# Performance work log

Hardware: AMD Instinct MI355X
Metric: run time of the kernel (lower is better)

## Reference

```python
import jax, jax.numpy as jnp
import numpy as np

FIELD_DIMS = [1000000, 100000, 1008, 1004, 102, 1000, 500, 50, 112, 107]
B = 16384
EMB = 32
DENSE = 16
MLP = [256, 128, 64]
BN_EPS = 1e-5
V_TOTAL = int(np.sum(FIELD_DIMS))
OFFSETS = jnp.asarray(np.concatenate([[0], np.cumsum(FIELD_DIMS)[:-1]]), dtype=jnp.int64)


def _xavier(key, fan_out, fan_in):
    lim = float(np.sqrt(6.0 / (fan_in + fan_out)))
    return jax.random.uniform(key, (fan_out, fan_in), jnp.float32, -lim, lim)


def setup_inputs() -> dict:
    key = jax.random.key(0)
    ks = jax.random.split(key, 16)
    # per-field in-range indices, stacked to [B, n_fields]
    sparse_cols = [jax.random.randint(jax.random.fold_in(ks[0], i), (B,), 0, d)
                   for i, d in enumerate(FIELD_DIMS)]
    sparse_inputs = jnp.stack(sparse_cols, axis=1).astype(jnp.int64)
    dense_inputs = jax.random.normal(ks[1], (B, DENSE), jnp.float32)
    # concatenated embedding / first-order bias tables (same math as per-field nn.Embedding)
    emb_table = 0.01 * jax.random.normal(ks[2], (V_TOTAL, EMB), jnp.float32)
    bias_table = 0.01 * jax.random.normal(ks[3], (V_TOTAL, 1), jnp.float32)
    fm_bias = jnp.zeros((1,), jnp.float32)
    dims = [len(FIELD_DIMS) * EMB + DENSE] + MLP
    params = {}
    for li in range(len(MLP)):
        params[f"W{li}"] = _xavier(ks[4 + li], dims[li + 1], dims[li])
        params[f"b{li}"] = jnp.zeros((dims[li + 1],), jnp.float32)
        params[f"g{li}"] = jnp.ones((dims[li + 1],), jnp.float32)
        params[f"be{li}"] = jnp.zeros((dims[li + 1],), jnp.float32)
    Wo = _xavier(ks[10], 1, MLP[-1])
    bo = jnp.zeros((1,), jnp.float32)
    return dict(sparse_inputs=sparse_inputs, dense_inputs=dense_inputs,
                emb_table=emb_table, bias_table=bias_table, fm_bias=fm_bias,
                Wo=Wo, bo=bo, **params)


def reference(sparse_inputs, dense_inputs, emb_table, bias_table, fm_bias,
              Wo, bo, W0, b0, g0, be0, W1, b1, g1, be1, W2, b2, g2, be2):
    idx = sparse_inputs + OFFSETS[None, :]           # [B, F] global rows
    field_embs = emb_table[idx]                      # [B, F, E] multi-table gather
    # FM first order: sum of per-field scalar biases
    fm_first = bias_table[idx][..., 0].sum(axis=1)   # [B]
    # FM second order: 0.5 * sum_d ((sum_f e)^2 - sum_f e^2)
    s = field_embs.sum(axis=1)                       # [B, E]
    sq = (field_embs * field_embs).sum(axis=1)       # [B, E]
    fm_second = 0.5 * (s * s - sq).sum(axis=-1)      # [B]
    fm_out = fm_bias[0] + fm_first + fm_second
    # deep component (BatchNorm in eval mode at init stats: mean=0, var=1; dropout=identity)
    x = jnp.concatenate([field_embs.reshape(field_embs.shape[0], -1), dense_inputs], axis=-1)
    inv = 1.0 / jnp.sqrt(1.0 + BN_EPS)
    for W, b, g, be in ((W0, b0, g0, be0), (W1, b1, g1, be1), (W2, b2, g2, be2)):
        h = x @ W.T + b
        h = h * (g * inv) + be
        x = jax.nn.relu(h)
    deep_out = (x @ Wo.T + bo)[:, 0]
    return jax.nn.sigmoid(fm_out + deep_out)
```

## Files before the change

### kernel.cpp

```cpp
#include <hip/hip_runtime.h>
#include <hip/hip_bf16.h>
#include <math.h>

#define BROWS 16384
#define NF    10
#define EMB   32
#define DENSE 16
#define K0S   352
#define K0    336
#define N0    256
#define N1    128
#define N2    64
#define BN_INV 0.99999500003749969f

__constant__ int c_offsets[NF] = {
    0, 1000000, 1100000, 1101008, 1102012,
    1102114, 1103114, 1103614, 1103664, 1103776
};

typedef short  bf16x8 __attribute__((ext_vector_type(8)));
typedef float  f32x4  __attribute__((ext_vector_type(4)));

union Frag { bf16x8 v; unsigned u[4]; };

static __device__ __forceinline__ unsigned short f2bf(float x) {
    union { float f; unsigned u; } c; c.f = x;
    unsigned r = (c.u + 0x7FFFu + ((c.u >> 16) & 1u)) >> 16;
    return (unsigned short)r;
}
static __device__ __forceinline__ unsigned pk2(float x, float y) {
    __hip_bfloat162 h = __float22bfloat162_rn(make_float2(x, y));
    union { __hip_bfloat162 h; unsigned u; } c; c.h = h; return c.u;
}

__global__ __launch_bounds__(256) void k_wconv_all(
    const float* __restrict__ W0, const float* __restrict__ W1,
    const float* __restrict__ W2,
    unsigned short* __restrict__ W0b, unsigned short* __restrict__ W1b,
    unsigned short* __restrict__ W2b)
{
    int i = blockIdx.x * 256 + threadIdx.x;
    if (i < N0 * K0S) {
        int r = i / K0S, c = i - r * K0S;
        W0b[i] = f2bf(c < K0 ? W0[r * K0 + c] : 0.f);
    } else if (i < N0 * K0S + N1 * N0) {
        int j = i - N0 * K0S;
        W1b[j] = f2bf(W1[j]);
    } else {
        int j = i - (N0 * K0S + N1 * N0);
        W2b[j] = f2bf(W2[j]);
    }
}

__global__ __launch_bounds__(256) void k_fused_all(
    const int*   __restrict__ sparse,
    const float* __restrict__ dense,
    const float* __restrict__ emb,
    const float* __restrict__ bias_tab,
    const float* __restrict__ fm_bias,
    const unsigned short* __restrict__ W0b,
    const float* __restrict__ b0, const float* __restrict__ g0,
    const float* __restrict__ be0,
    const unsigned short* __restrict__ W1b,
    const float* __restrict__ b1, const float* __restrict__ g1,
    const float* __restrict__ be1,
    const unsigned short* __restrict__ W2b,
    const float* __restrict__ b2, const float* __restrict__ g2,
    const float* __restrict__ be2,
    const float* __restrict__ Wo,
    const float* __restrict__ bo,
    float* __restrict__ out)
{
    __shared__ unsigned short x1s[32][N0 + 2];
    __shared__ unsigned short h2s[32][N1 + 2];
    __shared__ float fmld[32];
    __shared__ float partial[2][32];

    const int tid  = threadIdx.x;
    const int wave = tid >> 6;
    const int lane = tid & 63;
    const int l16  = lane & 15;
    const int quad = lane >> 4;
    const int rg   = wave & 1;
    const int hh   = wave >> 1;
    const int bm   = blockIdx.x * 32;
    const int arow = bm + rg * 16 + l16;

    int idx[NF];
#pragma unroll
    for (int f = 0; f < NF; ++f)
        idx[f] = sparse[arow * NF + f] + c_offsets[f];

    float first = 0.f, sq = 0.f;
    float s8[8];
#pragma unroll
    for (int j = 0; j < 8; ++j) s8[j] = 0.f;

    if (hh == 0) {
#pragma unroll
        for (int f = 0; f < NF; ++f)
            if ((f & 3) == quad) first += bias_tab[idx[f]];
    }

    f32x4 acc1[8];
#pragma unroll
    for (int nt = 0; nt < 8; ++nt) acc1[nt] = (f32x4){0.f, 0.f, 0.f, 0.f};

    const unsigned short* wp0 = W0b + (size_t)(hh * 128 + l16) * K0S + quad * 8;

#pragma unroll
    for (int f = 0; f < NF; ++f) {
        const float4* ep = (const float4*)(emb + (size_t)idx[f] * EMB) + quad * 2;
        float4 v0 = ep[0];
        float4 v1 = ep[1];
        if (hh == 0) {
            s8[0] += v0.x; s8[1] += v0.y; s8[2] += v0.z; s8[3] += v0.w;
            s8[4] += v1.x; s8[5] += v1.y; s8[6] += v1.z; s8[7] += v1.w;
            sq += v0.x*v0.x + v0.y*v0.y + v0.z*v0.z + v0.w*v0.w
                + v1.x*v1.x + v1.y*v1.y + v1.z*v1.z + v1.w*v1.w;
        }
        Frag a;
        a.u[0] = pk2(v0.x, v0.y); a.u[1] = pk2(v0.z, v0.w);
        a.u[2] = pk2(v1.x, v1.y); a.u[3] = pk2(v1.z, v1.w);
#pragma unroll
        for (int nt = 0; nt < 8; ++nt) {
            bf16x8 w = *(const bf16x8*)(wp0 + (size_t)(nt * 16) * K0S + f * 32);
            acc1[nt] = __builtin_amdgcn_mfma_f32_16x16x32_bf16(a.v, w, acc1[nt], 0, 0, 0);
        }
    }
    {
        Frag a;
        if (quad < 2) {
            const float4* dp = (const float4*)(dense + arow * DENSE) + quad * 2;
            float4 v0 = dp[0];
            float4 v1 = dp[1];
            a.u[0] = pk2(v0.x, v0.y); a.u[1] = pk2(v0.z, v0.w);
            a.u[2] = pk2(v1.x, v1.y); a.u[3] = pk2(v1.z, v1.w);
        } else {
            a.u[0] = 0; a.u[1] = 0; a.u[2] = 0; a.u[3] = 0;
        }
#pragma unroll
        for (int nt = 0; nt < 8; ++nt) {
            bf16x8 w = *(const bf16x8*)(wp0 + (size_t)(nt * 16) * K0S + 320);
            acc1[nt] = __builtin_amdgcn_mfma_f32_16x16x32_bf16(a.v, w, acc1[nt], 0, 0, 0);
        }
    }

    if (hh == 0) {
        float ss = 0.f;
#pragma unroll
        for (int j = 0; j < 8; ++j) ss += s8[j] * s8[j];
        ss += __shfl_xor(ss, 16); ss += __shfl_xor(ss, 32);
        sq += __shfl_xor(sq, 16); sq += __shfl_xor(sq, 32);
        first += __shfl_xor(first, 16); first += __shfl_xor(first, 32);
        if (quad == 0)
            fmld[rg * 16 + l16] = fm_bias[0] + first + 0.5f * (ss - sq);
    }

#pragma unroll
    for (int nt = 0; nt < 8; ++nt) {
        int col = hh * 128 + nt * 16 + l16;
        float sc = g0[col] * BN_INV;
        float tb = fmaf(b0[col], sc, be0[col]);
#pragma unroll
        for (int r = 0; r < 4; ++r) {
            float v = fmaf(acc1[nt][r], sc, tb);
            v = v > 0.f ? v : 0.f;
            x1s[rg * 16 + quad * 4 + r][col] = f2bf(v);
        }
    }
    __syncthreads();

    f32x4 acc2[4];
#pragma unroll
    for (int nt = 0; nt < 4; ++nt) acc2[nt] = (f32x4){0.f, 0.f, 0.f, 0.f};
    const unsigned short* wp1 = W1b + (size_t)(hh * 64 + l16) * N0 + quad * 8;
#pragma unroll
    for (int ks = 0; ks < 8; ++ks) {
        bf16x8 a = *(const bf16x8*)(&x1s[rg * 16 + l16][ks * 32 + quad * 8]);
#pragma unroll
        for (int nt = 0; nt < 4; ++nt) {
            bf16x8 w = *(const bf16x8*)(wp1 + (size_t)(nt * 16) * N0 + ks * 32);
            acc2[nt] = __builtin_amdgcn_mfma_f32_16x16x32_bf16(a, w, acc2[nt], 0, 0, 0);
        }
    }
#pragma unroll
    for (int nt = 0; nt < 4; ++nt) {
        int col = hh * 64 + nt * 16 + l16;
        float sc = g1[col] * BN_INV;
        float tb = fmaf(b1[col], sc, be1[col]);
#pragma unroll
        for (int r = 0; r < 4; ++r) {
            float v = fmaf(acc2[nt][r], sc, tb);
            v = v > 0.f ? v : 0.f;
            h2s[rg * 16 + quad * 4 + r][col] = f2bf(v);
        }
    }
    __syncthreads();

    f32x4 acc3[2];
#pragma unroll
    for (int nt = 0; nt < 2; ++nt) acc3[nt] = (f32x4){0.f, 0.f, 0.f, 0.f};
    const unsigned short* wp2 = W2b + (size_t)(hh * 32 + l16) * N1 + quad * 8;
#pragma unroll
    for (int ks = 0; ks < 4; ++ks) {
        bf16x8 a = *(const bf16x8*)(&h2s[rg * 16 + l16][ks * 32 + quad * 8]);
#pragma unroll
        for (int nt = 0; nt < 2; ++nt) {
            bf16x8 w = *(const bf16x8*)(wp2 + (size_t)(nt * 16) * N1 + ks * 32);
            acc3[nt] = __builtin_amdgcn_mfma_f32_16x16x32_bf16(a, w, acc3[nt], 0, 0, 0);
        }
    }

    float p[4] = {0.f, 0.f, 0.f, 0.f};
#pragma unroll
    for (int nt = 0; nt < 2; ++nt) {
        int col = hh * 32 + nt * 16 + l16;
        float sc = g2[col] * BN_INV;
        float tb = fmaf(b2[col], sc, be2[col]);
        float wo = Wo[col];
#pragma unroll
        for (int r = 0; r < 4; ++r) {
            float v = fmaf(acc3[nt][r], sc, tb);
            v = v > 0.f ? v : 0.f;
            p[r] = fmaf(v, wo, p[r]);
        }
    }
#pragma unroll
    for (int r = 0; r < 4; ++r) {
        p[r] += __shfl_xor(p[r], 1);
        p[r] += __shfl_xor(p[r], 2);
        p[r] += __shfl_xor(p[r], 4);
        p[r] += __shfl_xor(p[r], 8);
    }
    if (l16 == 0) {
#pragma unroll
        for (int r = 0; r < 4; ++r)
            partial[hh][rg * 16 + quad * 4 + r] = p[r];
    }
    __syncthreads();

    if (tid < 32) {
        float z = fmld[tid] + partial[0][tid] + partial[1][tid] + bo[0];
        out[bm + tid] = 1.f / (1.f + expf(-z));
    }
}

extern "C" void kernel_launch(void* const* d_in, const int* in_sizes, int n_in,
                              void* d_out, int out_size, void* d_ws, size_t ws_size,
                              hipStream_t stream)
{
    const int*   sparse   = (const int*)  d_in[0];
    const float* dense    = (const float*)d_in[1];
    const float* emb      = (const float*)d_in[2];
    const float* bias_tab = (const float*)d_in[3];
    const float* fm_bias  = (const float*)d_in[4];
    const float* Wo       = (const float*)d_in[5];
    const float* bo       = (const float*)d_in[6];
    const float* W0 = (const float*)d_in[7];
    const float* b0 = (const float*)d_in[8];
    const float* g0 = (const float*)d_in[9];
    const float* be0= (const float*)d_in[10];
    const float* W1 = (const float*)d_in[11];
    const float* b1 = (const float*)d_in[12];
    const float* g1 = (const float*)d_in[13];
    const float* be1= (const float*)d_in[14];
    const float* W2 = (const float*)d_in[15];
    const float* b2 = (const float*)d_in[16];
    const float* g2 = (const float*)d_in[17];
    const float* be2= (const float*)d_in[18];

    float* out = (float*)d_out;

    char* p = (char*)d_ws;
    unsigned short* W0b = (unsigned short*)p; p += (size_t)N0 * K0S * 2;
    unsigned short* W1b = (unsigned short*)p; p += (size_t)N1 * N0 * 2;
    unsigned short* W2b = (unsigned short*)p; p += (size_t)N2 * N1 * 2;

    k_wconv_all<<<(N0 * K0S + N1 * N0 + N2 * N1) / 256, 256, 0, stream>>>(
        W0, W1, W2, W0b, W1b, W2b);

    k_fused_all<<<BROWS / 32, 256, 0, stream>>>(
        sparse, dense, emb, bias_tab, fm_bias,
        W0b, b0, g0, be0, W1b, b1, g1, be1, W2b, b2, g2, be2,
        Wo, bo, out);
}
```

Before: 234.6 us.

## Stage gathered embeddings in LDS and split MLP columns across four waves

The block first gathers all 32 rows' embeddings into a shared bf16 A tile, using coalesced float4 loads driven by indices held in shared memory. The FM terms are then computed from that tile, and each of the four waves handles a quarter of the output columns for both 16-row groups. Before, two waves redundantly gathered the same embeddings and loaded disjoint halves of the weights. Now each embedding row is fetched once and each weight fragment is reused across 32 rows, at the cost of extra LDS traffic and syncs. The FM second-order term is now computed from bf16-rounded embeddings, which slightly reduces its precision.

New measurement: 230.9 us. Within noise of the previous version (-1.6%).

```diff
diff --git a/kernel.cpp b/kernel.cpp
--- a/kernel.cpp
+++ b/kernel.cpp
@@ -21,8 +21,6 @@
 typedef short  bf16x8 __attribute__((ext_vector_type(8)));
 typedef float  f32x4  __attribute__((ext_vector_type(4)));
 
-union Frag { bf16x8 v; unsigned u[4]; };
-
 static __device__ __forceinline__ unsigned short f2bf(float x) {
     union { float f; unsigned u; } c; c.f = x;
     unsigned r = (c.u + 0x7FFFu + ((c.u >> 16) & 1u)) >> 16;
@@ -31,6 +29,9 @@
 static __device__ __forceinline__ unsigned pk2(float x, float y) {
     __hip_bfloat162 h = __float22bfloat162_rn(make_float2(x, y));
     union { __hip_bfloat162 h; unsigned u; } c; c.h = h; return c.u;
+}
+static __device__ __forceinline__ float bf2f(unsigned short h) {
+    union { unsigned u; float f; } c; c.u = (unsigned)h << 16; return c.f;
 }
 
 __global__ __launch_bounds__(256) void k_wconv_all(
@@ -71,177 +72,205 @@
     const float* __restrict__ bo,
     float* __restrict__ out)
 {
-    __shared__ unsigned short x1s[32][N0 + 2];
-    __shared__ unsigned short h2s[32][N1 + 2];
+    __shared__ unsigned short As[32][360];
+    __shared__ unsigned short x1s[32][264];
+    __shared__ unsigned short h2s[32][136];
+    __shared__ int   gidx[32][NF];
+    __shared__ float biasp[32][NF];
     __shared__ float fmld[32];
-    __shared__ float partial[2][32];
-
-    const int tid  = threadIdx.x;
-    const int wave = tid >> 6;
+    __shared__ float partial[4][32];
+
+    const int tid = threadIdx.x;
+    const int bm  = blockIdx.x * 32;
+
+#pragma unroll
+    for (int i = 0; i < 2; ++i) {
+        int p = tid + (i << 8);
+        if (p < 320) {
+            int row = p / NF, f = p - row * NF;
+            int g = sparse[bm * NF + p] + c_offsets[f];
+            gidx[row][f]  = g;
+            biasp[row][f] = bias_tab[g];
+        }
+        {
+            int row = p >> 4, d = p & 15;
+            As[row][320 + d] = f2bf(dense[bm * DENSE + p]);
+            As[row][336 + d] = 0;
+        }
+    }
+    __syncthreads();
+
+#pragma unroll
+    for (int i = 0; i < 10; ++i) {
+        int c   = tid + (i << 8);
+        int row = c / 80;
+        int rem = c - row * 80;
+        int f   = rem >> 3, sub = rem & 7;
+        const float4 v = *(const float4*)(emb + (size_t)gidx[row][f] * EMB + (sub << 2));
+        uint2 pk; pk.x = pk2(v.x, v.y); pk.y = pk2(v.z, v.w);
+        *(uint2*)&As[row][(f << 5) + (sub << 2)] = pk;
+    }
+    __syncthreads();
+
+    {
+        const int rowA = tid >> 5;
+        const int e    = tid & 31;
+        float s0 = 0.f, q0 = 0.f, s1 = 0.f, q1 = 0.f;
+        float s2 = 0.f, q2 = 0.f, s3 = 0.f, q3 = 0.f;
+#pragma unroll
+        for (int f = 0; f < NF; ++f) {
+            float a = bf2f(As[rowA     ][(f << 5) + e]);
+            float b = bf2f(As[rowA +  8][(f << 5) + e]);
+            float c = bf2f(As[rowA + 16][(f << 5) + e]);
+            float d = bf2f(As[rowA + 24][(f << 5) + e]);
+            s0 += a; q0 += a * a;
+            s1 += b; q1 += b * b;
+            s2 += c; q2 += c * c;
+            s3 += d; q3 += d * d;
+        }
+        float r0 = 0.5f * (s0 * s0 - q0);
+        float r1 = 0.5f * (s1 * s1 - q1);
+        float r2 = 0.5f * (s2 * s2 - q2);
+        float r3 = 0.5f * (s3 * s3 - q3);
+        if (e < NF) {
+            r0 += biasp[rowA     ][e];
+            r1 += biasp[rowA +  8][e];
+            r2 += biasp[rowA + 16][e];
+            r3 += biasp[rowA + 24][e];
+        }
+#pragma unroll
+        for (int m = 1; m < 32; m <<= 1) {
+            r0 += __shfl_xor(r0, m); r1 += __shfl_xor(r1, m);
+            r2 += __shfl_xor(r2, m); r3 += __shfl_xor(r3, m);
+        }
+        if (e == 0) {
+            float fb = fm_bias[0];
+            fmld[rowA     ] = fb + r0;
+            fmld[rowA +  8] = fb + r1;
+            fmld[rowA + 16] = fb + r2;
+            fmld[rowA + 24] = fb + r3;
+        }
+    }
+
     const int lane = tid & 63;
     const int l16  = lane & 15;
     const int quad = lane >> 4;
-    const int rg   = wave & 1;
-    const int hh   = wave >> 1;
-    const int bm   = blockIdx.x * 32;
-    const int arow = bm + rg * 16 + l16;
-
-    int idx[NF];
-#pragma unroll
-    for (int f = 0; f < NF; ++f)
-        idx[f] = sparse[arow * NF + f] + c_offsets[f];
-
-    float first = 0.f, sq = 0.f;
-    float s8[8];
-#pragma unroll
-    for (int j = 0; j < 8; ++j) s8[j] = 0.f;
-
-    if (hh == 0) {
-#pragma unroll
-        for (int f = 0; f < NF; ++f)
-            if ((f & 3) == quad) first += bias_tab[idx[f]];
-    }
-
-    f32x4 acc1[8];
-#pragma unroll
-    for (int nt = 0; nt < 8; ++nt) acc1[nt] = (f32x4){0.f, 0.f, 0.f, 0.f};
-
-    const unsigned short* wp0 = W0b + (size_t)(hh * 128 + l16) * K0S + quad * 8;
-
-#pragma unroll
-    for (int f = 0; f < NF; ++f) {
-        const float4* ep = (const float4*)(emb + (size_t)idx[f] * EMB) + quad * 2;
-        float4 v0 = ep[0];
-        float4 v1 = ep[1];
-        if (hh == 0) {
-            s8[0] += v0.x; s8[1] += v0.y; s8[2] += v0.z; s8[3] += v0.w;
-            s8[4] += v1.x; s8[5] += v1.y; s8[6] += v1.z; s8[7] += v1.w;
-            sq += v0.x*v0.x + v0.y*v0.y + v0.z*v0.z + v0.w*v0.w
-                + v1.x*v1.x + v1.y*v1.y + v1.z*v1.z + v1.w*v1.w;
-        }
-        Frag a;
-        a.u[0] = pk2(v0.x, v0.y); a.u[1] = pk2(v0.z, v0.w);
-        a.u[2] = pk2(v1.x, v1.y); a.u[3] = pk2(v1.z, v1.w);
-#pragma unroll
-        for (int nt = 0; nt < 8; ++nt) {
-            bf16x8 w = *(const bf16x8*)(wp0 + (size_t)(nt * 16) * K0S + f * 32);
-            acc1[nt] = __builtin_amdgcn_mfma_f32_16x16x32_bf16(a.v, w, acc1[nt], 0, 0, 0);
-        }
-    }
-    {
-        Frag a;
-        if (quad < 2) {
-            const float4* dp = (const float4*)(dense + arow * DENSE) + quad * 2;
-            float4 v0 = dp[0];
-            float4 v1 = dp[1];
-            a.u[0] = pk2(v0.x, v0.y); a.u[1] = pk2(v0.z, v0.w);
-            a.u[2] = pk2(v1.x, v1.y); a.u[3] = pk2(v1.z, v1.w);
-        } else {
-            a.u[0] = 0; a.u[1] = 0; a.u[2] = 0; a.u[3] = 0;
-        }
-#pragma unroll
-        for (int nt = 0; nt < 8; ++nt) {
-            bf16x8 w = *(const bf16x8*)(wp0 + (size_t)(nt * 16) * K0S + 320);
-            acc1[nt] = __builtin_amdgcn_mfma_f32_16x16x32_bf16(a.v, w, acc1[nt], 0, 0, 0);
-        }
-    }
-
-    if (hh == 0) {
-        float ss = 0.f;
-#pragma unroll
-        for (int j = 0; j < 8; ++j) ss += s8[j] * s8[j];
-        ss += __shfl_xor(ss, 16); ss += __shfl_xor(ss, 32);
-        sq += __shfl_xor(sq, 16); sq += __shfl_xor(sq, 32);
-        first += __shfl_xor(first, 16); first += __shfl_xor(first, 32);
-        if (quad == 0)
-            fmld[rg * 16 + l16] = fm_bias[0] + first + 0.5f * (ss - sq);
-    }
-
-#pragma unroll
-    for (int nt = 0; nt < 8; ++nt) {
-        int col = hh * 128 + nt * 16 + l16;
+    const int hh   = tid >> 6;
+
+    f32x4 acc1[2][4];
+#pragma unroll
+    for (int rg = 0; rg < 2; ++rg)
+#pragma unroll
+        for (int nt = 0; nt < 4; ++nt) acc1[rg][nt] = (f32x4){0.f, 0.f, 0.f, 0.f};
+
+    const unsigned short* wp0 = W0b + (size_t)(hh * 64 + l16) * K0S + quad * 8;
+#pragma unroll
+    for (int ks = 0; ks < 11; ++ks) {
+        bf16x8 a0 = *(const bf16x8*)&As[l16     ][(ks << 5) + (quad << 3)];
+        bf16x8 a1 = *(const bf16x8*)&As[l16 + 16][(ks << 5) + (quad << 3)];
+#pragma unroll
+        for (int nt = 0; nt < 4; ++nt) {
+            bf16x8 w = *(const bf16x8*)(wp0 + (size_t)(nt * 16) * K0S + ks * 32);
+            acc1[0][nt] = __builtin_amdgcn_mfma_f32_16x16x32_bf16(a0, w, acc1[0][nt], 0, 0, 0);
+            acc1[1][nt] = __builtin_amdgcn_mfma_f32_16x16x32_bf16(a1, w, acc1[1][nt], 0, 0, 0);
+        }
+    }
+#pragma unroll
+    for (int nt = 0; nt < 4; ++nt) {
+        int col = hh * 64 + nt * 16 + l16;
         float sc = g0[col] * BN_INV;
         float tb = fmaf(b0[col], sc, be0[col]);
 #pragma unroll
-        for (int r = 0; r < 4; ++r) {
-            float v = fmaf(acc1[nt][r], sc, tb);
-            v = v > 0.f ? v : 0.f;
-            x1s[rg * 16 + quad * 4 + r][col] = f2bf(v);
-        }
-    }
-    __syncthreads();
-
-    f32x4 acc2[4];
-#pragma unroll
-    for (int nt = 0; nt < 4; ++nt) acc2[nt] = (f32x4){0.f, 0.f, 0.f, 0.f};
-    const unsigned short* wp1 = W1b + (size_t)(hh * 64 + l16) * N0 + quad * 8;
+        for (int rg = 0; rg < 2; ++rg)
+#pragma unroll
+            for (int r = 0; r < 4; ++r) {
+                float v = fmaf(acc1[rg][nt][r], sc, tb);
+                v = v > 0.f ? v : 0.f;
+                x1s[rg * 16 + quad * 4 + r][col] = f2bf(v);
+            }
+    }
+    __syncthreads();
+
+    f32x4 acc2[2][2];
+#pragma unroll
+    for (int rg = 0; rg < 2; ++rg)
+#pragma unroll
+        for (int nt = 0; nt < 2; ++nt) acc2[rg][nt] = (f32x4){0.f, 0.f, 0.f, 0.f};
+
+    const unsigned short* wp1 = W1b + (size_t)(hh * 32 + l16) * N0 + quad * 8;
 #pragma unroll
     for (int ks = 0; ks < 8; ++ks) {
-        bf16x8 a = *(const bf16x8*)(&x1s[rg * 16 + l16][ks * 32 + quad * 8]);
-#pragma unroll
-        for (int nt = 0; nt < 4; ++nt) {
+        bf16x8 a0 = *(const bf16x8*)&x1s[l16     ][(ks << 5) + (quad << 3)];
+        bf16x8 a1 = *(const bf16x8*)&x1s[l16 + 16][(ks << 5) + (quad << 3)];
+#pragma unroll
+        for (int nt = 0; nt < 2; ++nt) {
             bf16x8 w = *(const bf16x8*)(wp1 + (size_t)(nt * 16) * N0 + ks * 32);
-            acc2[nt] = __builtin_amdgcn_mfma_f32_16x16x32_bf16(a, w, acc2[nt], 0, 0, 0);
-        }
-    }
-#pragma unroll
-    for (int nt = 0; nt < 4; ++nt) {
-        int col = hh * 64 + nt * 16 + l16;
+            acc2[0][nt] = __builtin_amdgcn_mfma_f32_16x16x32_bf16(a0, w, acc2[0][nt], 0, 0, 0);
+            acc2[1][nt] = __builtin_amdgcn_mfma_f32_16x16x32_bf16(a1, w, acc2[1][nt], 0, 0, 0);
+        }
+    }
+#pragma unroll
+    for (int nt = 0; nt < 2; ++nt) {
+        int col = hh * 32 + nt * 16 + l16;
         float sc = g1[col] * BN_INV;
         float tb = fmaf(b1[col], sc, be1[col]);
 #pragma unroll
-        for (int r = 0; r < 4; ++r) {
-            float v = fmaf(acc2[nt][r], sc, tb);
-            v = v > 0.f ? v : 0.f;
-            h2s[rg * 16 + quad * 4 + r][col] = f2bf(v);
-        }
+        for (int rg = 0; rg < 2; ++rg)
+#pragma unroll
+            for (int r = 0; r < 4; ++r) {
+                float v = fmaf(acc2[rg][nt][r], sc, tb);
+                v = v > 0.f ? v : 0.f;
+                h2s[rg * 16 + quad * 4 + r][col] = f2bf(v);
+            }
     }
     __syncthreads();
 
     f32x4 acc3[2];
-#pragma unroll
-    for (int nt = 0; nt < 2; ++nt) acc3[nt] = (f32x4){0.f, 0.f, 0.f, 0.f};
-    const unsigned short* wp2 = W2b + (size_t)(hh * 32 + l16) * N1 + quad * 8;
+    acc3[0] = (f32x4){0.f, 0.f, 0.f, 0.f};
+    acc3[1] = (f32x4){0.f, 0.f, 0.f, 0.f};
+    const unsigned short* wp2 = W2b + (size_t)(hh * 16 + l16) * N1 + quad * 8;
 #pragma unroll
     for (int ks = 0; ks < 4; ++ks) {
-        bf16x8 a = *(const bf16x8*)(&h2s[rg * 16 + l16][ks * 32 + quad * 8]);
-#pragma unroll
-        for (int nt = 0; nt < 2; ++nt) {
-            bf16x8 w = *(const bf16x8*)(wp2 + (size_t)(nt * 16) * N1 + ks * 32);
-            acc3[nt] = __builtin_amdgcn_mfma_f32_16x16x32_bf16(a, w, acc3[nt], 0, 0, 0);
-        }
-    }
-
-    float p[4] = {0.f, 0.f, 0.f, 0.f};
-#pragma unroll
-    for (int nt = 0; nt < 2; ++nt) {
-        int col = hh * 32 + nt * 16 + l16;
+        bf16x8 a0 = *(const bf16x8*)&h2s[l16     ][(ks << 5) + (quad << 3)];
+        bf16x8 a1 = *(const bf16x8*)&h2s[l16 + 16][(ks << 5) + (quad << 3)];
+        bf16x8 w  = *(const bf16x8*)(wp2 + ks * 32);
+        acc3[0] = __builtin_amdgcn_mfma_f32_16x16x32_bf16(a0, w, acc3[0], 0, 0, 0);
+        acc3[1] = __builtin_amdgcn_mfma_f32_16x16x32_bf16(a1, w, acc3[1], 0, 0, 0);
+    }
+
+    {
+        int col = hh * 16 + l16;
         float sc = g2[col] * BN_INV;
         float tb = fmaf(b2[col], sc, be2[col]);
         float wo = Wo[col];
+        float p0[4], p1[4];
 #pragma unroll
         for (int r = 0; r < 4; ++r) {
-            float v = fmaf(acc3[nt][r], sc, tb);
-            v = v > 0.f ? v : 0.f;
-            p[r] = fmaf(v, wo, p[r]);
-        }
-    }
-#pragma unroll
-    for (int r = 0; r < 4; ++r) {
-        p[r] += __shfl_xor(p[r], 1);
-        p[r] += __shfl_xor(p[r], 2);
-        p[r] += __shfl_xor(p[r], 4);
-        p[r] += __shfl_xor(p[r], 8);
-    }
-    if (l16 == 0) {
-#pragma unroll
-        for (int r = 0; r < 4; ++r)
-            partial[hh][rg * 16 + quad * 4 + r] = p[r];
+            float v0 = fmaf(acc3[0][r], sc, tb); v0 = v0 > 0.f ? v0 : 0.f;
+            float v1 = fmaf(acc3[1][r], sc, tb); v1 = v1 > 0.f ? v1 : 0.f;
+            p0[r] = v0 * wo;
+            p1[r] = v1 * wo;
+        }
+#pragma unroll
+        for (int r = 0; r < 4; ++r) {
+            p0[r] += __shfl_xor(p0[r], 1); p0[r] += __shfl_xor(p0[r], 2);
+            p0[r] += __shfl_xor(p0[r], 4); p0[r] += __shfl_xor(p0[r], 8);
+            p1[r] += __shfl_xor(p1[r], 1); p1[r] += __shfl_xor(p1[r], 2);
+            p1[r] += __shfl_xor(p1[r], 4); p1[r] += __shfl_xor(p1[r], 8);
+        }
+        if (l16 == 0) {
+#pragma unroll
+            for (int r = 0; r < 4; ++r) {
+                partial[hh][     quad * 4 + r] = p0[r];
+                partial[hh][16 + quad * 4 + r] = p1[r];
+            }
+        }
     }
     __syncthreads();
 
     if (tid < 32) {
-        float z = fmld[tid] + partial[0][tid] + partial[1][tid] + bo[0];
+        float z = fmld[tid] + partial[0][tid] + partial[1][tid]
+                + partial[2][tid] + partial[3][tid] + bo[0];
         out[bm + tid] = 1.f / (1.f + expf(-z));
     }
 }
```
